# Kernel tuning notes

Hardware: AMD Instinct MI355X
Metric: run time of the kernel (lower is better)

Reference implementation:

```python
import jax, jax.numpy as jnp
import numpy as np


def setup_inputs() -> dict:
    key = jax.random.key(0)
    k1, k2, k3, k4 = jax.random.split(key, 4)
    bs, seq_len, num_heads, head_dim, num_pages = 16, 4096, 16, 128, 32768
    q = jax.random.normal(k1, (bs, num_heads, 1, head_dim), dtype=jnp.float32)
    kv_cache = jax.random.normal(k2, (2, num_pages, num_heads, head_dim), dtype=jnp.float32)
    k_indices = jax.random.randint(k3, (bs, seq_len), 0, num_pages, dtype=jnp.int64)
    v_indices = jax.random.randint(k4, (bs, seq_len), 0, num_pages, dtype=jnp.int64)
    return {"q": q, "kv_cache": kv_cache, "k_indices": k_indices, "v_indices": v_indices}


def reference(q, kv_cache, k_indices, v_indices):
    # Gather per-token K/V rows from the paged cache.
    k_cache = kv_cache[0]                      # [P, H, D]
    v_cache = kv_cache[1]                      # [P, H, D]
    k = k_cache[k_indices]                     # [B, S, H, D]
    v = v_cache[v_indices]                     # [B, S, H, D]
    head_dim = q.shape[-1]
    scale = 1.0 / jnp.sqrt(jnp.asarray(head_dim, dtype=q.dtype))
    # scores: [B, H, Q, S] (Q == 1 for decode); SDPA default: no mask, non-causal.
    scores = jnp.einsum("bhqd,bshd->bhqs", q, k) * scale
    probs = jax.nn.softmax(scores, axis=-1)
    out = jnp.einsum("bhqs,bshd->bhqd", probs, v)  # [B, H, Q, D]
    return out
```

## Files before the change

### kernel.cpp

```cpp
#include <hip/hip_runtime.h>

#define B 16
#define S 4096
#define H 16
#define D 128
#define P 32768
#define HD 2048
#define NSPLIT 8
#define TOKW 128
#define SCALE 0.08838834764831845f

#define O_E 0
#define O_PART (B * H * S)

__global__ __launch_bounds__(256) void kphase(
    const float* __restrict__ q, const float* __restrict__ kv,
    const int* __restrict__ kidx, float* __restrict__ ws)
{
    const int split = blockIdx.x, h = blockIdx.y, b = blockIdx.z;
    const int wave = threadIdx.x >> 6, lane = threadIdx.x & 63;

    const float2 qv = *reinterpret_cast<const float2*>(
        q + ((size_t)b * H + h) * D + lane * 2);

    const int s0 = split * (S / NSPLIT) + wave * TOKW;
    const int myk0 = kidx[b * S + s0 + lane];
    const int myk1 = kidx[b * S + s0 + 64 + lane];

    float e0 = 0.f, e1 = 0.f;
    int kp = __shfl(myk0, 0);
    float2 kr = *reinterpret_cast<const float2*>(
        kv + (size_t)kp * HD + h * D + lane * 2);
    float2 krn = kr;

    for (int t = 0; t < TOKW; ++t) {
        if (t + 1 < TOKW) {
            const int tn = t + 1;
            const int kpn = (tn < 64) ? __shfl(myk0, tn) : __shfl(myk1, tn - 64);
            krn = *reinterpret_cast<const float2*>(
                kv + (size_t)kpn * HD + h * D + lane * 2);
        }
        float dot = qv.x * kr.x + qv.y * kr.y;
        #pragma unroll
        for (int o = 32; o > 0; o >>= 1) dot += __shfl_xor(dot, o);
        const float e = __expf(dot * SCALE);
        if (t == lane)      e0 = e;
        if (t == 64 + lane) e1 = e;
        kr = krn;
    }

    float* eb = ws + O_E + ((size_t)b * H + h) * S + s0;
    eb[lane]      = e0;
    eb[64 + lane] = e1;
}

__global__ __launch_bounds__(256) void vphase(
    const float* __restrict__ kv, const int* __restrict__ vidx,
    float* __restrict__ ws)
{
    const int split = blockIdx.x, h = blockIdx.y, b = blockIdx.z;
    const int wave = threadIdx.x >> 6, lane = threadIdx.x & 63;
    const float* vbase = kv + (size_t)P * HD;

    const int s0 = split * (S / NSPLIT) + wave * TOKW;
    const int myv0 = vidx[b * S + s0 + lane];
    const int myv1 = vidx[b * S + s0 + 64 + lane];

    const float* eb = ws + O_E + ((size_t)b * H + h) * S + s0;
    const float e0 = eb[lane];
    const float e1 = eb[64 + lane];

    float2 acc = make_float2(0.f, 0.f);
    int vp = __shfl(myv0, 0);
    float2 vr = *reinterpret_cast<const float2*>(
        vbase + (size_t)vp * HD + h * D + lane * 2);
    float2 vrn = vr;

    for (int t = 0; t < TOKW; ++t) {
        if (t + 1 < TOKW) {
            const int tn = t + 1;
            const int vpn = (tn < 64) ? __shfl(myv0, tn) : __shfl(myv1, tn - 64);
            vrn = *reinterpret_cast<const float2*>(
                vbase + (size_t)vpn * HD + h * D + lane * 2);
        }
        const float et = (t < 64) ? __shfl(e0, t) : __shfl(e1, t - 64);
        acc.x += et * vr.x;
        acc.y += et * vr.y;
        vr = vrn;
    }

    __shared__ float lds_acc[4][D];
    __shared__ float lds_l[4];
    lds_acc[wave][lane * 2]     = acc.x;
    lds_acc[wave][lane * 2 + 1] = acc.y;
    float lsum = e0 + e1;
    #pragma unroll
    for (int o = 32; o > 0; o >>= 1) lsum += __shfl_xor(lsum, o);
    if (lane == 0) lds_l[wave] = lsum;
    __syncthreads();

    if (threadIdx.x < D) {
        const int d = threadIdx.x;
        float* outp = ws + O_PART +
                      ((size_t)(b * H + h) * NSPLIT + split) * (D + 1);
        const float a = lds_acc[0][d] + lds_acc[1][d] +
                        lds_acc[2][d] + lds_acc[3][d];
        outp[d] = a;
        if (d == 0) outp[D] = lds_l[0] + lds_l[1] + lds_l[2] + lds_l[3];
    }
}

__global__ __launch_bounds__(128) void pa_reduce(
    const float* __restrict__ ws, float* __restrict__ out)
{
    const int bh = blockIdx.x;
    const int d  = threadIdx.x;
    const float* base = ws + O_PART + (size_t)bh * NSPLIT * (D + 1);

    float L = 0.f, a = 0.f;
    #pragma unroll
    for (int i = 0; i < NSPLIT; ++i) {
        L += base[i * (D + 1) + D];
        a += base[i * (D + 1) + d];
    }
    out[(size_t)bh * D + d] = a / L;
}

extern "C" void kernel_launch(void* const* d_in, const int* in_sizes, int n_in,
                              void* d_out, int out_size, void* d_ws, size_t ws_size,
                              hipStream_t stream) {
    const float* q    = (const float*)d_in[0];
    const float* kv   = (const float*)d_in[1];
    const int*   kidx = (const int*)d_in[2];
    const int*   vidx = (const int*)d_in[3];
    float*       out  = (float*)d_out;
    float*       ws   = (float*)d_ws;

    dim3 grid(NSPLIT, H, B);
    kphase   <<<grid, 256, 0, stream>>>(q, kv, kidx, ws);
    vphase   <<<grid, 256, 0, stream>>>(kv, vidx, ws);
    pa_reduce<<<B * H, 128, 0, stream>>>(ws, out);
}
```

Before: 177.2 us.

## Fuse K and V phases into one kernel with half-wave token pairs

Merges the separate score and value kernels into a single pass that computes exp-scores and accumulates weighted V in the same loop. This removes the intermediate score buffer round-trip and one launch. Each wave now splits into two 32-lane halves, each handling a different token with float4 loads, so every iteration keeps two K and two V row loads in flight. The halves are combined with a cross-half shuffle at the end. Skipping max subtraction in softmax is kept from the earlier code.

```diff
diff --git a/kernel.cpp b/kernel.cpp
--- a/kernel.cpp
+++ b/kernel.cpp
@@ -10,99 +10,79 @@
 #define TOKW 128
 #define SCALE 0.08838834764831845f
 
-#define O_E 0
-#define O_PART (B * H * S)
 
-__global__ __launch_bounds__(256) void kphase(
+__global__ __launch_bounds__(256) void pa_main(
     const float* __restrict__ q, const float* __restrict__ kv,
-    const int* __restrict__ kidx, float* __restrict__ ws)
+    const int* __restrict__ kidx, const int* __restrict__ vidx,
+    float* __restrict__ ws)
 {
     const int split = blockIdx.x, h = blockIdx.y, b = blockIdx.z;
     const int wave = threadIdx.x >> 6, lane = threadIdx.x & 63;
+    const int dc = lane & 31;
+    const float* vbase = kv + (size_t)P * HD;
 
-    const float2 qv = *reinterpret_cast<const float2*>(
-        q + ((size_t)b * H + h) * D + lane * 2);
+    const float4 qv = *reinterpret_cast<const float4*>(
+        q + ((size_t)b * H + h) * D + dc * 4);
 
     const int s0 = split * (S / NSPLIT) + wave * TOKW;
     const int myk0 = kidx[b * S + s0 + lane];
     const int myk1 = kidx[b * S + s0 + 64 + lane];
-
-    float e0 = 0.f, e1 = 0.f;
-    int kp = __shfl(myk0, 0);
-    float2 kr = *reinterpret_cast<const float2*>(
-        kv + (size_t)kp * HD + h * D + lane * 2);
-    float2 krn = kr;
-
-    for (int t = 0; t < TOKW; ++t) {
-        if (t + 1 < TOKW) {
-            const int tn = t + 1;
-            const int kpn = (tn < 64) ? __shfl(myk0, tn) : __shfl(myk1, tn - 64);
-            krn = *reinterpret_cast<const float2*>(
-                kv + (size_t)kpn * HD + h * D + lane * 2);
-        }
-        float dot = qv.x * kr.x + qv.y * kr.y;
-        #pragma unroll
-        for (int o = 32; o > 0; o >>= 1) dot += __shfl_xor(dot, o);
-        const float e = __expf(dot * SCALE);
-        if (t == lane)      e0 = e;
-        if (t == 64 + lane) e1 = e;
-        kr = krn;
-    }
-
-    float* eb = ws + O_E + ((size_t)b * H + h) * S + s0;
-    eb[lane]      = e0;
-    eb[64 + lane] = e1;
-}
-
-__global__ __launch_bounds__(256) void vphase(
-    const float* __restrict__ kv, const int* __restrict__ vidx,
-    float* __restrict__ ws)
-{
-    const int split = blockIdx.x, h = blockIdx.y, b = blockIdx.z;
-    const int wave = threadIdx.x >> 6, lane = threadIdx.x & 63;
-    const float* vbase = kv + (size_t)P * HD;
-
-    const int s0 = split * (S / NSPLIT) + wave * TOKW;
     const int myv0 = vidx[b * S + s0 + lane];
     const int myv1 = vidx[b * S + s0 + 64 + lane];
 
-    const float* eb = ws + O_E + ((size_t)b * H + h) * S + s0;
-    const float e0 = eb[lane];
-    const float e1 = eb[64 + lane];
+    const unsigned hoff = h * D + dc * 4;
+    const bool loA = (lane < 32);
 
-    float2 acc = make_float2(0.f, 0.f);
-    int vp = __shfl(myv0, 0);
-    float2 vr = *reinterpret_cast<const float2*>(
-        vbase + (size_t)vp * HD + h * D + lane * 2);
-    float2 vrn = vr;
+    float4 acc = make_float4(0.f, 0.f, 0.f, 0.f);
+    float lsum = 0.f;
 
-    for (int t = 0; t < TOKW; ++t) {
-        if (t + 1 < TOKW) {
-            const int tn = t + 1;
-            const int vpn = (tn < 64) ? __shfl(myv0, tn) : __shfl(myv1, tn - 64);
-            vrn = *reinterpret_cast<const float2*>(
-                vbase + (size_t)vpn * HD + h * D + lane * 2);
+    {
+        const int kA = __shfl(myk0, 0), kB = __shfl(myk1, 0);
+        const int vA = __shfl(myv0, 0), vB = __shfl(myv1, 0);
+        const int kp = loA ? kA : kB;
+        const int vp = loA ? vA : vB;
+        acc = acc;
+        float4 kr0 = *(const float4*)(kv + (size_t)(unsigned)kp * HD + hoff);
+        float4 vr0 = *(const float4*)(vbase + (size_t)(unsigned)vp * HD + hoff);
+        float4 kr = kr0, vr = vr0;
+
+        for (int t = 0; t < 64; ++t) {
+            float4 krn = kr, vrn = vr;
+            if (t + 1 < 64) {
+                const int kAn = __shfl(myk0, t + 1), kBn = __shfl(myk1, t + 1);
+                const int vAn = __shfl(myv0, t + 1), vBn = __shfl(myv1, t + 1);
+                const int kn = loA ? kAn : kBn;
+                const int vn = loA ? vAn : vBn;
+                krn = *(const float4*)(kv + (size_t)(unsigned)kn * HD + hoff);
+                vrn = *(const float4*)(vbase + (size_t)(unsigned)vn * HD + hoff);
+            }
+            float dot = qv.x * kr.x + qv.y * kr.y + qv.z * kr.z + qv.w * kr.w;
+            #pragma unroll
+            for (int o = 16; o > 0; o >>= 1) dot += __shfl_xor(dot, o);
+            const float e = __expf(dot * SCALE);
+            lsum += e;
+            acc.x += e * vr.x; acc.y += e * vr.y;
+            acc.z += e * vr.z; acc.w += e * vr.w;
+            kr = krn; vr = vrn;
         }
-        const float et = (t < 64) ? __shfl(e0, t) : __shfl(e1, t - 64);
-        acc.x += et * vr.x;
-        acc.y += et * vr.y;
-        vr = vrn;
     }
+
+    acc.x += __shfl_xor(acc.x, 32);
+    acc.y += __shfl_xor(acc.y, 32);
+    acc.z += __shfl_xor(acc.z, 32);
+    acc.w += __shfl_xor(acc.w, 32);
+    lsum  += __shfl_xor(lsum, 32);
 
     __shared__ float lds_acc[4][D];
     __shared__ float lds_l[4];
-    lds_acc[wave][lane * 2]     = acc.x;
-    lds_acc[wave][lane * 2 + 1] = acc.y;
-    float lsum = e0 + e1;
-    #pragma unroll
-    for (int o = 32; o > 0; o >>= 1) lsum += __shfl_xor(lsum, o);
+    if (lane < 32)
+        *reinterpret_cast<float4*>(&lds_acc[wave][dc * 4]) = acc;
     if (lane == 0) lds_l[wave] = lsum;
     __syncthreads();
 
     if (threadIdx.x < D) {
         const int d = threadIdx.x;
-        float* outp = ws + O_PART +
-                      ((size_t)(b * H + h) * NSPLIT + split) * (D + 1);
+        float* outp = ws + ((size_t)(b * H + h) * NSPLIT + split) * (D + 1);
         const float a = lds_acc[0][d] + lds_acc[1][d] +
                         lds_acc[2][d] + lds_acc[3][d];
         outp[d] = a;
@@ -115,7 +95,7 @@
 {
     const int bh = blockIdx.x;
     const int d  = threadIdx.x;
-    const float* base = ws + O_PART + (size_t)bh * NSPLIT * (D + 1);
+    const float* base = ws + (size_t)bh * NSPLIT * (D + 1);
 
     float L = 0.f, a = 0.f;
     #pragma unroll
@@ -137,7 +117,6 @@
     float*       ws   = (float*)d_ws;
 
     dim3 grid(NSPLIT, H, B);
-    kphase   <<<grid, 256, 0, stream>>>(q, kv, kidx, ws);
-    vphase   <<<grid, 256, 0, stream>>>(kv, vidx, ws);
+    pa_main  <<<grid, 256, 0, stream>>>(q, kv, kidx, vidx, ws);
     pa_reduce<<<B * H, 128, 0, stream>>>(ws, out);
 }
```

New measurement: 156.2 us. 11.9% less time.
